# Kernel optimization log

Measured on AMD Instinct MI355X. Metric: run time of the kernel, lower is better.

## Reference

```python
import jax, jax.numpy as jnp
import numpy as np

B, Q, K = 16, 8192, 8192
D_QK, D_V = 64, 64      # raw query/key and value feature dims
H = 8                    # num_heads
DP = 128                 # proj_qks output dim (per default MLP [128, 128])
VP = 64                  # proj_vs output dim (per default MLP [128, 64])
LN_EPS = 1e-6            # flax LayerNorm default


def setup_inputs() -> dict:
    key = jax.random.key(0)
    ks_ = jax.random.split(key, 12)
    f = lambda k, s: jax.random.normal(k, s, jnp.float32)
    return {
        "qs": f(ks_[0], (B, Q, D_QK)),
        "ks": f(ks_[1], (B, K, D_QK)),
        "vs": f(ks_[2], (B, K, D_V)),
        "qs_s": f(ks_[3], (B, Q, D_QK)),
        "ks_s": f(ks_[4], (B, K, D_QK)),
        "valid_lens": jax.random.randint(ks_[5], (B,), 1, K + 1, jnp.int32),
        # proj_qks = MLP([128, 128], gelu): Dense(128) -> gelu -> Dense(128)
        "Wq1": f(ks_[6], (2 * D_QK, DP)) / np.sqrt(2 * D_QK).astype(np.float32),
        "bq1": jnp.zeros((DP,), jnp.float32),
        "Wq2": f(ks_[7], (DP, DP)) / np.sqrt(DP).astype(np.float32),
        "bq2": jnp.zeros((DP,), jnp.float32),
        # proj_vs = MLP([128, 64], gelu): Dense(128) -> gelu -> Dense(64)
        "Wv1": f(ks_[8], (D_V, DP)) / np.sqrt(D_V).astype(np.float32),
        "bv1": jnp.zeros((DP,), jnp.float32),
        "Wv2": f(ks_[9], (DP, VP)) / np.sqrt(DP).astype(np.float32),
        "bv2": jnp.zeros((VP,), jnp.float32),
        "ln_scale": jnp.ones((VP,), jnp.float32),
        "ln_bias": jnp.zeros((VP,), jnp.float32),
    }


def _mlp2(x, W1, b1, W2, b2):
    # Dense -> gelu (tanh approx, flax default) -> Dense
    return jax.nn.gelu(x @ W1 + b1) @ W2 + b2


def reference(qs, ks, vs, qs_s, ks_s, valid_lens,
              Wq1, bq1, Wq2, bq2, Wv1, bv1, Wv2, bv2,
              ln_scale, ln_bias):
    Kl, D = ks.shape[-2], ks.shape[-1]  # D taken BEFORE stacking, as in source
    scale = D ** 0.25
    # stack spatial features then feature-map MLPs
    q = _mlp2(jnp.concatenate([qs_s, qs], axis=-1), Wq1, bq1, Wq2, bq2) / scale
    k = _mlp2(jnp.concatenate([ks_s, ks], axis=-1), Wq1, bq1, Wq2, bq2) / scale
    v = _mlp2(vs, Wv1, bv1, Wv2, bv2)
    # valid-length masking of keys, mean-style normalization of values
    mask = (jnp.arange(Kl)[None, :] < valid_lens[:, None]).astype(k.dtype)[..., None]
    k = k * mask
    v = v / valid_lens[:, None, None].astype(v.dtype)
    Bn, Qn = q.shape[0], q.shape[1]
    q = q.reshape(Bn, Qn, H, DP // H)   # B Q H d
    k = k.reshape(Bn, Kl, H, DP // H)   # B K H d
    v = v.reshape(Bn, Kl, H, VP // H)   # B K H e
    # linear attention: KV outer-product summary then apply queries
    kv = jnp.einsum('bkhd,bkhe->bhde', k, v)          # B H d e
    ctx = jnp.einsum('bqhd,bhde->bqhe', q, kv)        # B Q H e
    ctx = ctx.reshape(Bn, Qn, VP)
    # LayerNorm over last dim
    mu = ctx.mean(-1, keepdims=True)
    var = ((ctx - mu) ** 2).mean(-1, keepdims=True)
    return (ctx - mu) * jax.lax.rsqrt(var + LN_EPS) * ln_scale + ln_bias
```

## Files before the change

kernel.cpp:

```cpp
#include <hip/hip_runtime.h>
#include <hip/hip_bf16.h>


typedef __attribute__((ext_vector_type(8))) short short8;
typedef __attribute__((ext_vector_type(4))) float f32x4;
typedef unsigned int u32;
typedef unsigned short u16;

#define MFMA(A,B,C) __builtin_amdgcn_mfma_f32_16x16x32_bf16((A),(B),(C),0,0,0)
#define SBAR() __builtin_amdgcn_sched_barrier(0)

#define LDH 136
#define LDT 40
#define INVS 0.3535533905932738f

__device__ __forceinline__ u16 bfc(float x){
  __hip_bfloat16 h = __float2bfloat16(x);
  return __bfloat16_as_ushort(h);
}
__device__ __forceinline__ u32 pack2(float a, float b){
  return (u32)bfc(a) | ((u32)bfc(b) << 16);
}
__device__ __forceinline__ float b2f(u16 w){
  return __uint_as_float(((u32)w) << 16);
}
__device__ __forceinline__ short8 cvt8(f32x4 lo, f32x4 hi){
  short8 r;
  r[0]=(short)bfc(lo[0]); r[1]=(short)bfc(lo[1]);
  r[2]=(short)bfc(lo[2]); r[3]=(short)bfc(lo[3]);
  r[4]=(short)bfc(hi[0]); r[5]=(short)bfc(hi[1]);
  r[6]=(short)bfc(hi[2]); r[7]=(short)bfc(hi[3]);
  return r;
}
__device__ __forceinline__ float gelu_f(float x){
  float s = x*x;
  float u = x * __builtin_fmaf(s, 0.035677408136300125f, 0.7978845608028654f);
  float e = __builtin_amdgcn_exp2f(u * -2.885390081777927f);
  return x * __builtin_amdgcn_rcpf(1.0f + e);
}

__global__ void dk_prep(const float* __restrict__ Wq1, const float* __restrict__ Wq2,
                        const float* __restrict__ Wv1, const float* __restrict__ Wv2,
                        u16* __restrict__ wt){
  int i = blockIdx.x*256 + threadIdx.x;
  int e = i & 7;
  int lane = (i >> 3) & 63;
  int chunk = i >> 9;
  int c = lane & 15, g = lane >> 4;
  int k0 = 8*g + e;
  float v;
  if (chunk < 32){
    int mt = chunk >> 2, ks4 = chunk & 3;
    v = Wq1[(ks4*32 + k0)*128 + mt*16 + c];
  } else if (chunk < 64){
    int ch = chunk - 32; int mt = ch >> 2, ks4 = ch & 3;
    v = Wq2[(ks4*32 + k0)*128 + mt*16 + c] * INVS;
  } else if (chunk < 80){
    int ch = chunk - 64; int mt = ch >> 1, ks2 = ch & 1;
    v = Wv1[(ks2*32 + k0)*128 + mt*16 + c];
  } else {
    int ch = chunk - 80; int n2 = ch >> 2, ks4 = ch & 3;
    v = Wv2[(ks4*32 + k0)*64 + n2*16 + c];
  }
  wt[i] = bfc(v);
}

__global__ __launch_bounds__(128, 2) void dk_stage1(
    const float* __restrict__ ksp, const float* __restrict__ kssp,
    const float* __restrict__ vsp, const int* __restrict__ vlen,
    const float* __restrict__ bq1, const float* __restrict__ bq2,
    const float* __restrict__ bv1, const float* __restrict__ bv2,
    const u16* __restrict__ wt, float* __restrict__ kvgr, int repmask)
{
  __shared__ u16 sA[2][5120];
  __shared__ u16 sB[2][2560];
  const int tid = threadIdx.x;
  const int w = tid >> 6, l = tid & 63;
  const int c = l & 15, g = l >> 4;

  int pfx = (l < 16) ? ((vlen[l] + 63) >> 6) : 0;
  #pragma unroll
  for (int m=1; m<16; m<<=1){
    int v = __shfl_up(pfx, m, 64);
    if (l >= m) pfx += v;
  }
  const int T = __shfl(pfx, 15, 64);
  const int t = blockIdx.x;
  if (t >= T) return;
  unsigned long long mk = __ballot(l < 16 && pfx <= t);
  const int b = __popcll(mk);
  const int jb = t - (b ? __shfl(pfx, b-1, 64) : 0);
  const int len = vlen[b];
  const int rbase = jb*64 + w*32;
  if (rbase >= len) return;
  const int rep = t & repmask;
  const size_t row0 = (size_t)b*8192 + rbase;

  u16* H1 = sA[w];
  u16* KT = sA[w];
  u16* VT = sB[w];
  const u16* Wq1t = wt;
  const u16* Wq2t = wt + 16384;
  const u16* Wv1t = wt + 32768;
  const u16* Wv2t = wt + 40960;
  const f32x4 z4 = {0.f,0.f,0.f,0.f};

  {
    f32x4 xvf[8];
    #pragma unroll
    for (int ks2=0; ks2<2; ++ks2){
      #pragma unroll
      for (int nt=0; nt<2; ++nt){
        const float* src = vsp + (row0 + nt*16 + c)*64 + ks2*32 + 8*g;
        xvf[(ks2*2+nt)*2+0] = *(const f32x4*)src;
        xvf[(ks2*2+nt)*2+1] = *(const f32x4*)(src+4);
      }
    }
    SBAR();
    short8 xv[2][2];
    #pragma unroll
    for (int ks2=0; ks2<2; ++ks2)
      #pragma unroll
      for (int nt=0; nt<2; ++nt)
        xv[ks2][nt] = cvt8(xvf[(ks2*2+nt)*2+0], xvf[(ks2*2+nt)*2+1]);
    f32x4 av[8][2];
    #pragma unroll
    for (int mt=0; mt<8; ++mt){ av[mt][0]=z4; av[mt][1]=z4; }
    #pragma unroll
    for (int ks2=0; ks2<2; ++ks2){
      short8 wa[8];
      #pragma unroll
      for (int mt=0; mt<8; ++mt)
        wa[mt] = *(const short8*)&Wv1t[((mt*2+ks2)*64 + l)*8];
      SBAR();
      #pragma unroll
      for (int mt=0; mt<8; ++mt){
        av[mt][0] = MFMA(wa[mt], xv[ks2][0], av[mt][0]);
        av[mt][1] = MFMA(wa[mt], xv[ks2][1], av[mt][1]);
      }
    }
    #pragma unroll
    for (int mt=0; mt<8; ++mt){
      const f32x4 bia = *(const f32x4*)&bv1[mt*16 + 4*g];
      #pragma unroll
      for (int nt=0; nt<2; ++nt){
        uint2 pp;
        pp.x = pack2(gelu_f(av[mt][nt][0]+bia[0]), gelu_f(av[mt][nt][1]+bia[1]));
        pp.y = pack2(gelu_f(av[mt][nt][2]+bia[2]), gelu_f(av[mt][nt][3]+bia[3]));
        *(uint2*)&H1[(nt*16 + c)*LDH + mt*16 + 4*g] = pp;
      }
    }
  }
  {
    f32x4 acv[2][4];
    #pragma unroll
    for (int n2=0; n2<4; ++n2){ acv[0][n2]=z4; acv[1][n2]=z4; }
    #pragma unroll
    for (int ks4=0; ks4<4; ++ks4){
      short8 wb[4];
      #pragma unroll
      for (int n2=0; n2<4; ++n2)
        wb[n2] = *(const short8*)&Wv2t[((n2*4+ks4)*64 + l)*8];
      SBAR();
      const short8 ah0 = *(const short8*)&H1[(c     )*LDH + ks4*32 + 8*g];
      const short8 ah1 = *(const short8*)&H1[(16 + c)*LDH + ks4*32 + 8*g];
      #pragma unroll
      for (int n2=0; n2<4; ++n2){
        acv[0][n2] = MFMA(ah0, wb[n2], acv[0][n2]);
        acv[1][n2] = MFMA(ah1, wb[n2], acv[1][n2]);
      }
    }
    #pragma unroll
    for (int n2=0; n2<4; ++n2){
      const float bb = bv2[n2*16 + c];
      #pragma unroll
      for (int mt=0; mt<2; ++mt){
        uint2 pp;
        pp.x = pack2(acv[mt][n2][0]+bb, acv[mt][n2][1]+bb);
        pp.y = pack2(acv[mt][n2][2]+bb, acv[mt][n2][3]+bb);
        *(uint2*)&VT[(n2*16+c)*LDT + mt*16 + 4*g] = pp;
      }
    }
  }
  {
    f32x4 xkf[16];
    #pragma unroll
    for (int ks4=0; ks4<4; ++ks4){
      #pragma unroll
      for (int nt=0; nt<2; ++nt){
        const int kk = ks4*32 + 8*g;
        const float* src = (ks4 < 2) ? (kssp + (row0 + nt*16 + c)*64 + kk)
                                     : (ksp  + (row0 + nt*16 + c)*64 + (kk - 64));
        xkf[(ks4*2+nt)*2+0] = *(const f32x4*)src;
        xkf[(ks4*2+nt)*2+1] = *(const f32x4*)(src+4);
      }
    }
    SBAR();
    short8 xk[4][2];
    #pragma unroll
    for (int ks4=0; ks4<4; ++ks4)
      #pragma unroll
      for (int nt=0; nt<2; ++nt)
        xk[ks4][nt] = cvt8(xkf[(ks4*2+nt)*2+0], xkf[(ks4*2+nt)*2+1]);
    f32x4 acc[8][2];
    #pragma unroll
    for (int mt=0; mt<8; ++mt){ acc[mt][0]=z4; acc[mt][1]=z4; }
    #pragma unroll
    for (int ks4=0; ks4<4; ++ks4){
      short8 wa[8];
      #pragma unroll
      for (int mt=0; mt<8; ++mt)
        wa[mt] = *(const short8*)&Wq1t[((mt*4+ks4)*64 + l)*8];
      SBAR();
      #pragma unroll
      for (int mt=0; mt<8; ++mt){
        acc[mt][0] = MFMA(wa[mt], xk[ks4][0], acc[mt][0]);
        acc[mt][1] = MFMA(wa[mt], xk[ks4][1], acc[mt][1]);
      }
    }
    #pragma unroll
    for (int mt=0; mt<8; ++mt){
      const f32x4 bia = *(const f32x4*)&bq1[mt*16 + 4*g];
      #pragma unroll
      for (int nt=0; nt<2; ++nt){
        uint2 pp;
        pp.x = pack2(gelu_f(acc[mt][nt][0]+bia[0]), gelu_f(acc[mt][nt][1]+bia[1]));
        pp.y = pack2(gelu_f(acc[mt][nt][2]+bia[2]), gelu_f(acc[mt][nt][3]+bia[3]));
        *(uint2*)&H1[(nt*16 + c)*LDH + mt*16 + 4*g] = pp;
      }
    }
  }
  {
    f32x4 acc2[2][8];
    #pragma unroll
    for (int n2=0; n2<8; ++n2){ acc2[0][n2]=z4; acc2[1][n2]=z4; }
    #pragma unroll
    for (int ks4=0; ks4<4; ++ks4){
      short8 wb[8];
      #pragma unroll
      for (int n2=0; n2<8; ++n2)
        wb[n2] = *(const short8*)&Wq2t[((n2*4+ks4)*64 + l)*8];
      SBAR();
      const short8 ah0 = *(const short8*)&H1[(c     )*LDH + ks4*32 + 8*g];
      const short8 ah1 = *(const short8*)&H1[(16 + c)*LDH + ks4*32 + 8*g];
      #pragma unroll
      for (int n2=0; n2<8; ++n2){
        acc2[0][n2] = MFMA(ah0, wb[n2], acc2[0][n2]);
        acc2[1][n2] = MFMA(ah1, wb[n2], acc2[1][n2]);
      }
    }
    #pragma unroll
    for (int n2=0; n2<8; ++n2){
      const float bb = bq2[n2*16 + c] * INVS;
      #pragma unroll
      for (int mt=0; mt<2; ++mt){
        const int r0 = rbase + mt*16 + 4*g;
        float v0 = (r0+0 < len) ? acc2[mt][n2][0] + bb : 0.f;
        float v1 = (r0+1 < len) ? acc2[mt][n2][1] + bb : 0.f;
        float v2 = (r0+2 < len) ? acc2[mt][n2][2] + bb : 0.f;
        float v3 = (r0+3 < len) ? acc2[mt][n2][3] + bb : 0.f;
        uint2 pp; pp.x = pack2(v0,v1); pp.y = pack2(v2,v3);
        *(uint2*)&KT[(n2*16 + c)*LDT + mt*16 + 4*g] = pp;
      }
    }
  }
  {
    short8 zf = {0,0,0,0,0,0,0,0};
    f32x4 kvacc[8];
    #pragma unroll
    for (int h=0; h<8; ++h) kvacc[h] = z4;
    #pragma unroll
    for (int h=0; h<8; ++h){
      const short8 ka = *(const short8*)&KT[(h*16 + c)*LDT + 8*g];
      short8 vb = zf;
      if (c < 8) vb = *(const short8*)&VT[(h*8 + c)*LDT + 8*g];
      kvacc[h] = MFMA(ka, vb, kvacc[h]);
    }
    if (c < 8){
      float* kvg = kvgr + ((size_t)rep*16 + b)*1024;
      #pragma unroll
      for (int h=0; h<8; ++h){
        #pragma unroll
        for (int r=0; r<4; ++r)
          atomicAdd(&kvg[(h*16 + 4*g + r)*8 + c], kvacc[h][r]);
      }
    }
  }
}

__global__ void dk_mid(const float* __restrict__ kvgr, int nrep,
                       const int* __restrict__ vlen,
                       const float* __restrict__ bq2,
                       const u16* __restrict__ wt,
                       u16* __restrict__ Mt, float* __restrict__ c0g)
{
  __shared__ float kvs[1024];
  const int b = blockIdx.x, t = threadIdx.x;
  const float inv_len = 1.0f / (float)vlen[b];
  #pragma unroll
  for (int k=0; k<4; ++k){
    const int idx = t + 256*k;
    float s = 0.f;
    for (int r=0; r<nrep; ++r) s += kvgr[((size_t)r*16 + b)*1024 + idx];
    kvs[idx] = s * inv_len;
  }
  __syncthreads();
  for (int k=0; k<32; ++k){
    const int o = t + 256*k;
    const int e = o >> 7, j = o & 127;
    const int h = e >> 3, e8 = e & 7;
    const int ks4 = j >> 5, gg = (j >> 3) & 3, el = j & 7;
    float s = 0.f;
    #pragma unroll
    for (int d=0; d<16; ++d){
      const int od = h*16 + d;
      const u16 wv = wt[16384 + (((od>>4)*4 + ks4)*64 + gg*16 + (od&15))*8 + el];
      s += b2f(wv) * kvs[h*128 + d*8 + e8];
    }
    const int n3 = e >> 4, cc = e & 15;
    Mt[(size_t)b*8192 + ((n3*4 + ks4)*64 + gg*16 + cc)*8 + el] = bfc(s);
  }
  if (t < 64){
    const int e = t, h = e >> 3, e8 = e & 7;
    float s = 0.f;
    #pragma unroll
    for (int d=0; d<16; ++d)
      s += bq2[h*16+d] * INVS * kvs[h*128 + d*8 + e8];
    c0g[b*64 + e] = s;
  }
}

__global__ __launch_bounds__(128, 2) void dk_stage2(
    const float* __restrict__ qsp, const float* __restrict__ qssp,
    const float* __restrict__ bq1,
    const float* __restrict__ lnw_g, const float* __restrict__ lnb_g,
    const u16* __restrict__ wt, const u16* __restrict__ Mt,
    const float* __restrict__ c0g, float* __restrict__ outp)
{
  __shared__ u16 sH1[2][32*LDH];
  const int tid = threadIdx.x;
  const int w = tid >> 6, l = tid & 63;
  const int c = l & 15, g = l >> 4;
  const int b  = blockIdx.x >> 7;
  const int jb = blockIdx.x & 127;
  const int rbase = jb*64 + w*32;
  u16* H1 = sH1[w];
  const u16* Wq1t = wt;
  const size_t row0 = (size_t)b*8192 + rbase;
  const f32x4 z4 = {0.f,0.f,0.f,0.f};

  {
    f32x4 xqf[16];
    #pragma unroll
    for (int ks4=0; ks4<4; ++ks4){
      #pragma unroll
      for (int nt=0; nt<2; ++nt){
        const int kk = ks4*32 + 8*g;
        const float* src = (ks4 < 2) ? (qssp + (row0 + nt*16 + c)*64 + kk)
                                     : (qsp  + (row0 + nt*16 + c)*64 + (kk - 64));
        xqf[(ks4*2+nt)*2+0] = *(const f32x4*)src;
        xqf[(ks4*2+nt)*2+1] = *(const f32x4*)(src+4);
      }
    }
    SBAR();
    short8 xq[4][2];
    #pragma unroll
    for (int ks4=0; ks4<4; ++ks4)
      #pragma unroll
      for (int nt=0; nt<2; ++nt)
        xq[ks4][nt] = cvt8(xqf[(ks4*2+nt)*2+0], xqf[(ks4*2+nt)*2+1]);
    f32x4 acc[8][2];
    #pragma unroll
    for (int mt=0; mt<8; ++mt){ acc[mt][0]=z4; acc[mt][1]=z4; }
    #pragma unroll
    for (int ks4=0; ks4<4; ++ks4){
      short8 wa[8];
      #pragma unroll
      for (int mt=0; mt<8; ++mt)
        wa[mt] = *(const short8*)&Wq1t[((mt*4+ks4)*64 + l)*8];
      SBAR();
      #pragma unroll
      for (int mt=0; mt<8; ++mt){
        acc[mt][0] = MFMA(wa[mt], xq[ks4][0], acc[mt][0]);
        acc[mt][1] = MFMA(wa[mt], xq[ks4][1], acc[mt][1]);
      }
    }
    #pragma unroll
    for (int mt=0; mt<8; ++mt){
      const f32x4 bia = *(const f32x4*)&bq1[mt*16 + 4*g];
      #pragma unroll
      for (int nt=0; nt<2; ++nt){
        uint2 pp;
        pp.x = pack2(gelu_f(acc[mt][nt][0]+bia[0]), gelu_f(acc[mt][nt][1]+bia[1]));
        pp.y = pack2(gelu_f(acc[mt][nt][2]+bia[2]), gelu_f(acc[mt][nt][3]+bia[3]));
        *(uint2*)&H1[(nt*16 + c)*LDH + mt*16 + 4*g] = pp;
      }
    }
  }
  f32x4 acc3[2][4];
  #pragma unroll
  for (int n3=0; n3<4; ++n3){ acc3[0][n3]=z4; acc3[1][n3]=z4; }
  const u16* Mb = Mt + (size_t)b*8192;
  {
    short8 bm[16];
    #pragma unroll
    for (int ks4=0; ks4<4; ++ks4)
      #pragma unroll
      for (int n3=0; n3<4; ++n3)
        bm[ks4*4+n3] = *(const short8*)&Mb[((n3*4+ks4)*64 + l)*8];
    SBAR();
    #pragma unroll
    for (int ks4=0; ks4<4; ++ks4){
      const short8 aq0 = *(const short8*)&H1[(c     )*LDH + ks4*32 + 8*g];
      const short8 aq1 = *(const short8*)&H1[(16 + c)*LDH + ks4*32 + 8*g];
      #pragma unroll
      for (int n3=0; n3<4; ++n3){
        acc3[0][n3] = MFMA(aq0, bm[ks4*4+n3], acc3[0][n3]);
        acc3[1][n3] = MFMA(aq1, bm[ks4*4+n3], acc3[1][n3]);
      }
    }
  }
  float c0v[4];
  #pragma unroll
  for (int n3=0; n3<4; ++n3) c0v[n3] = c0g[b*64 + n3*16 + c];
  float lnw[4], lnb[4];
  #pragma unroll
  for (int n3=0; n3<4; ++n3){ lnw[n3] = lnw_g[n3*16 + c]; lnb[n3] = lnb_g[n3*16 + c]; }
  float* Tb = (float*)H1;
  #pragma unroll
  for (int mt=0; mt<2; ++mt){
    #pragma unroll
    for (int r=0; r<4; ++r){
      float s1 = 0.f, s2 = 0.f;
      #pragma unroll
      for (int n3=0; n3<4; ++n3){
        float v = acc3[mt][n3][r] + c0v[n3];
        s1 += v; s2 += v*v;
      }
      #pragma unroll
      for (int m=1; m<16; m<<=1){
        s1 += __shfl_xor(s1, m, 64);
        s2 += __shfl_xor(s2, m, 64);
      }
      const float mu = s1 * (1.0f/64.0f);
      const float var = s2 * (1.0f/64.0f) - mu*mu;
      const float rs = rsqrtf(var + 1e-6f);
      const int rloc = mt*16 + 4*g + r;
      #pragma unroll
      for (int n3=0; n3<4; ++n3)
        Tb[rloc*68 + n3*16 + c] = (acc3[mt][n3][r] + c0v[n3] - mu)*rs*lnw[n3] + lnb[n3];
    }
  }
  float* ob = outp + row0*64;
  #pragma unroll
  for (int i=0; i<8; ++i){
    const int row = i*4 + (l>>4);
    const f32x4 vv = *(const f32x4*)&Tb[row*68 + (l&15)*4];
    *(f32x4*)(ob + row*64 + (l&15)*4) = vv;
  }
}

extern "C" void kernel_launch(void* const* d_in, const int* in_sizes, int n_in,
                              void* d_out, int out_size, void* d_ws, size_t ws_size,
                              hipStream_t stream)
{
  const float* qs   = (const float*)d_in[0];
  const float* ks   = (const float*)d_in[1];
  const float* vs   = (const float*)d_in[2];
  const float* qs_s = (const float*)d_in[3];
  const float* ks_s = (const float*)d_in[4];
  const int*   vl   = (const int*)d_in[5];
  const float* Wq1  = (const float*)d_in[6];
  const float* bq1  = (const float*)d_in[7];
  const float* Wq2  = (const float*)d_in[8];
  const float* bq2  = (const float*)d_in[9];
  const float* Wv1  = (const float*)d_in[10];
  const float* bv1  = (const float*)d_in[11];
  const float* Wv2  = (const float*)d_in[12];
  const float* bv2  = (const float*)d_in[13];
  const float* lnw  = (const float*)d_in[14];
  const float* lnb  = (const float*)d_in[15];
  (void)in_sizes; (void)n_in; (void)out_size;

  const size_t fixed = 96*1024 + 256*1024 + 4096;
  int nrep = 4;
  while (nrep > 1 && (size_t)nrep*65536 + fixed > ws_size) nrep >>= 1;
  float* kvgr = (float*)d_ws;
  u16*   wt   = (u16*)((char*)d_ws + (size_t)nrep*65536);
  u16*   Mt   = (u16*)((char*)wt + 96*1024);
  float* c0   = (float*)((char*)Mt + 256*1024);

  hipMemsetAsync(kvgr, 0, (size_t)nrep*65536, stream);
  dk_prep<<<192, 256, 0, stream>>>(Wq1, Wq2, Wv1, Wv2, wt);
  dk_stage1<<<2048, 128, 0, stream>>>(ks, ks_s, vs, vl, bq1, bq2, bv1, bv2,
                                      wt, kvgr, nrep - 1);
  dk_mid<<<16, 256, 0, stream>>>(kvgr, nrep, vl, bq2, wt, Mt, c0);
  dk_stage2<<<2048, 128, 0, stream>>>(qs, qs_s, bq1, lnw, lnb, wt, Mt, c0,
                                      (float*)d_out);
}
```

Baseline: 92.17 us.

## Stage bf16 weight tiles in shared memory cooperatively per block

Both kernels now copy each weight matrix (Wv1/Wv2, then Wq1, then Wq2) from global memory into a 32KB shared buffer using both waves cooperatively. Each wave then reads its MFMA operand fragments from LDS instead of global/L2, which halves the per-block global weight traffic. In stage2 the loads of the M matrix are hoisted to the top to overlap with the input and weight loads. The early per-wave return was removed so that __syncthreads is safe. The cost is extra LDS use (lower occupancy headroom), extra barriers, and more register pressure from the staging buffers.

```diff
diff --git a/kernel.cpp b/kernel.cpp
--- a/kernel.cpp
+++ b/kernel.cpp
@@ -74,6 +74,7 @@
 {
   __shared__ u16 sA[2][5120];
   __shared__ u16 sB[2][2560];
+  __shared__ u16 sW[16384];
   const int tid = threadIdx.x;
   const int w = tid >> 6, l = tid & 63;
   const int c = l & 15, g = l >> 4;
@@ -92,20 +93,19 @@
   const int jb = t - (b ? __shfl(pfx, b-1, 64) : 0);
   const int len = vlen[b];
   const int rbase = jb*64 + w*32;
-  if (rbase >= len) return;
   const int rep = t & repmask;
   const size_t row0 = (size_t)b*8192 + rbase;
 
   u16* H1 = sA[w];
   u16* KT = sA[w];
   u16* VT = sB[w];
-  const u16* Wq1t = wt;
-  const u16* Wq2t = wt + 16384;
-  const u16* Wv1t = wt + 32768;
-  const u16* Wv2t = wt + 40960;
   const f32x4 z4 = {0.f,0.f,0.f,0.f};
 
   {
+    uint4 stg[16];
+    #pragma unroll
+    for (int j=0; j<16; ++j)
+      stg[j] = *(const uint4*)&wt[((size_t)(64 + j*2 + w)*64 + l)*8];
     f32x4 xvf[8];
     #pragma unroll
     for (int ks2=0; ks2<2; ++ks2){
@@ -117,6 +117,11 @@
       }
     }
     SBAR();
+    #pragma unroll
+    for (int j=0; j<16; ++j)
+      *(uint4*)&sW[((j*2 + w)*64 + l)*8] = stg[j];
+    __syncthreads();
+
     short8 xv[2][2];
     #pragma unroll
     for (int ks2=0; ks2<2; ++ks2)
@@ -131,7 +136,7 @@
       short8 wa[8];
       #pragma unroll
       for (int mt=0; mt<8; ++mt)
-        wa[mt] = *(const short8*)&Wv1t[((mt*2+ks2)*64 + l)*8];
+        wa[mt] = *(const short8*)&sW[((mt*2+ks2)*64 + l)*8];
       SBAR();
       #pragma unroll
       for (int mt=0; mt<8; ++mt){
@@ -150,8 +155,6 @@
         *(uint2*)&H1[(nt*16 + c)*LDH + mt*16 + 4*g] = pp;
       }
     }
-  }
-  {
     f32x4 acv[2][4];
     #pragma unroll
     for (int n2=0; n2<4; ++n2){ acv[0][n2]=z4; acv[1][n2]=z4; }
@@ -160,7 +163,7 @@
       short8 wb[4];
       #pragma unroll
       for (int n2=0; n2<4; ++n2)
-        wb[n2] = *(const short8*)&Wv2t[((n2*4+ks4)*64 + l)*8];
+        wb[n2] = *(const short8*)&sW[((16 + n2*4+ks4)*64 + l)*8];
       SBAR();
       const short8 ah0 = *(const short8*)&H1[(c     )*LDH + ks4*32 + 8*g];
       const short8 ah1 = *(const short8*)&H1[(16 + c)*LDH + ks4*32 + 8*g];
@@ -182,7 +185,14 @@
       }
     }
   }
+  __syncthreads();
+
+  short8 xk[4][2];
   {
+    uint4 stg[16];
+    #pragma unroll
+    for (int j=0; j<16; ++j)
+      stg[j] = *(const uint4*)&wt[((size_t)(j*2 + w)*64 + l)*8];
     f32x4 xkf[16];
     #pragma unroll
     for (int ks4=0; ks4<4; ++ks4){
@@ -196,7 +206,11 @@
       }
     }
     SBAR();
-    short8 xk[4][2];
+    #pragma unroll
+    for (int j=0; j<16; ++j)
+      *(uint4*)&sW[((j*2 + w)*64 + l)*8] = stg[j];
+    __syncthreads();
+
     #pragma unroll
     for (int ks4=0; ks4<4; ++ks4)
       #pragma unroll
@@ -210,7 +224,7 @@
       short8 wa[8];
       #pragma unroll
       for (int mt=0; mt<8; ++mt)
-        wa[mt] = *(const short8*)&Wq1t[((mt*4+ks4)*64 + l)*8];
+        wa[mt] = *(const short8*)&sW[((mt*4+ks4)*64 + l)*8];
       SBAR();
       #pragma unroll
       for (int mt=0; mt<8; ++mt){
@@ -230,7 +244,19 @@
       }
     }
   }
+  __syncthreads();
+
   {
+    uint4 stg[16];
+    #pragma unroll
+    for (int j=0; j<16; ++j)
+      stg[j] = *(const uint4*)&wt[((size_t)(32 + j*2 + w)*64 + l)*8];
+    SBAR();
+    #pragma unroll
+    for (int j=0; j<16; ++j)
+      *(uint4*)&sW[((j*2 + w)*64 + l)*8] = stg[j];
+    __syncthreads();
+
     f32x4 acc2[2][8];
     #pragma unroll
     for (int n2=0; n2<8; ++n2){ acc2[0][n2]=z4; acc2[1][n2]=z4; }
@@ -239,7 +265,7 @@
       short8 wb[8];
       #pragma unroll
       for (int n2=0; n2<8; ++n2)
-        wb[n2] = *(const short8*)&Wq2t[((n2*4+ks4)*64 + l)*8];
+        wb[n2] = *(const short8*)&sW[((n2*4+ks4)*64 + l)*8];
       SBAR();
       const short8 ah0 = *(const short8*)&H1[(c     )*LDH + ks4*32 + 8*g];
       const short8 ah1 = *(const short8*)&H1[(16 + c)*LDH + ks4*32 + 8*g];
@@ -263,8 +289,6 @@
         *(uint2*)&KT[(n2*16 + c)*LDT + mt*16 + 4*g] = pp;
       }
     }
-  }
-  {
     short8 zf = {0,0,0,0,0,0,0,0};
     f32x4 kvacc[8];
     #pragma unroll
@@ -338,6 +362,7 @@
     const float* __restrict__ c0g, float* __restrict__ outp)
 {
   __shared__ u16 sH1[2][32*LDH];
+  __shared__ u16 sW[16384];
   const int tid = threadIdx.x;
   const int w = tid >> 6, l = tid & 63;
   const int c = l & 15, g = l >> 4;
@@ -345,24 +370,39 @@
   const int jb = blockIdx.x & 127;
   const int rbase = jb*64 + w*32;
   u16* H1 = sH1[w];
-  const u16* Wq1t = wt;
   const size_t row0 = (size_t)b*8192 + rbase;
   const f32x4 z4 = {0.f,0.f,0.f,0.f};
+  const u16* Mb = Mt + (size_t)b*8192;
+
+  uint4 stg[16];
+  #pragma unroll
+  for (int j=0; j<16; ++j)
+    stg[j] = *(const uint4*)&wt[((size_t)(j*2 + w)*64 + l)*8];
+  f32x4 xqf[16];
+  #pragma unroll
+  for (int ks4=0; ks4<4; ++ks4){
+    #pragma unroll
+    for (int nt=0; nt<2; ++nt){
+      const int kk = ks4*32 + 8*g;
+      const float* src = (ks4 < 2) ? (qssp + (row0 + nt*16 + c)*64 + kk)
+                                   : (qsp  + (row0 + nt*16 + c)*64 + (kk - 64));
+      xqf[(ks4*2+nt)*2+0] = *(const f32x4*)src;
+      xqf[(ks4*2+nt)*2+1] = *(const f32x4*)(src+4);
+    }
+  }
+  short8 bm[16];
+  #pragma unroll
+  for (int ks4=0; ks4<4; ++ks4)
+    #pragma unroll
+    for (int n3=0; n3<4; ++n3)
+      bm[ks4*4+n3] = *(const short8*)&Mb[((n3*4+ks4)*64 + l)*8];
+  SBAR();
+  #pragma unroll
+  for (int j=0; j<16; ++j)
+    *(uint4*)&sW[((j*2 + w)*64 + l)*8] = stg[j];
+  __syncthreads();
 
   {
-    f32x4 xqf[16];
-    #pragma unroll
-    for (int ks4=0; ks4<4; ++ks4){
-      #pragma unroll
-      for (int nt=0; nt<2; ++nt){
-        const int kk = ks4*32 + 8*g;
-        const float* src = (ks4 < 2) ? (qssp + (row0 + nt*16 + c)*64 + kk)
-                                     : (qsp  + (row0 + nt*16 + c)*64 + (kk - 64));
-        xqf[(ks4*2+nt)*2+0] = *(const f32x4*)src;
-        xqf[(ks4*2+nt)*2+1] = *(const f32x4*)(src+4);
-      }
-    }
-    SBAR();
     short8 xq[4][2];
     #pragma unroll
     for (int ks4=0; ks4<4; ++ks4)
@@ -377,7 +417,7 @@
       short8 wa[8];
       #pragma unroll
       for (int mt=0; mt<8; ++mt)
-        wa[mt] = *(const short8*)&Wq1t[((mt*4+ks4)*64 + l)*8];
+        wa[mt] = *(const short8*)&sW[((mt*4+ks4)*64 + l)*8];
       SBAR();
       #pragma unroll
       for (int mt=0; mt<8; ++mt){
@@ -400,24 +440,14 @@
   f32x4 acc3[2][4];
   #pragma unroll
   for (int n3=0; n3<4; ++n3){ acc3[0][n3]=z4; acc3[1][n3]=z4; }
-  const u16* Mb = Mt + (size_t)b*8192;
-  {
-    short8 bm[16];
-    #pragma unroll
-    for (int ks4=0; ks4<4; ++ks4)
-      #pragma unroll
-      for (int n3=0; n3<4; ++n3)
-        bm[ks4*4+n3] = *(const short8*)&Mb[((n3*4+ks4)*64 + l)*8];
-    SBAR();
-    #pragma unroll
-    for (int ks4=0; ks4<4; ++ks4){
-      const short8 aq0 = *(const short8*)&H1[(c     )*LDH + ks4*32 + 8*g];
-      const short8 aq1 = *(const short8*)&H1[(16 + c)*LDH + ks4*32 + 8*g];
-      #pragma unroll
-      for (int n3=0; n3<4; ++n3){
-        acc3[0][n3] = MFMA(aq0, bm[ks4*4+n3], acc3[0][n3]);
-        acc3[1][n3] = MFMA(aq1, bm[ks4*4+n3], acc3[1][n3]);
-      }
+  #pragma unroll
+  for (int ks4=0; ks4<4; ++ks4){
+    const short8 aq0 = *(const short8*)&H1[(c     )*LDH + ks4*32 + 8*g];
+    const short8 aq1 = *(const short8*)&H1[(16 + c)*LDH + ks4*32 + 8*g];
+    #pragma unroll
+    for (int n3=0; n3<4; ++n3){
+      acc3[0][n3] = MFMA(aq0, bm[ks4*4+n3], acc3[0][n3]);
+      acc3[1][n3] = MFMA(aq1, bm[ks4*4+n3], acc3[1][n3]);
     }
   }
   float c0v[4];
```

Measured after the change: 126.9 us. +37.6%, slower.

## Stage MLP weights into LDS via double-buffered async global_load_lds

Applied to the files above, without the earlier changes.

Weight fragments used by the MFMA loops were read by every wave straight from global memory. They are now copied into a shared double buffer with global_load_lds, both waves of a block cooperating, and the next chunk is prefetched while the current one is consumed, in both stage1 and stage2. The packed weight layout in the prep kernel is reordered so each 8-chunk group is contiguous in consumption order, and the stage1 early exit for fully masked waves is dropped so block-wide barriers stay valid. This adds several __syncthreads per tile and 16KB of LDS per block, which may reduce occupancy, and masked waves now do redundant work.

```diff
diff --git a/kernel.cpp b/kernel.cpp
--- a/kernel.cpp
+++ b/kernel.cpp
@@ -38,6 +38,19 @@
   float e = __builtin_amdgcn_exp2f(u * -2.885390081777927f);
   return x * __builtin_amdgcn_rcpf(1.0f + e);
 }
+__device__ __forceinline__ void gld_lds16(const u16* gsrc, u16* ldst){
+  __builtin_amdgcn_global_load_lds(
+      (const __attribute__((address_space(1))) void*)gsrc,
+      (__attribute__((address_space(3))) void*)ldst, 16, 0, 0);
+}
+__device__ __forceinline__ void stage8(const u16* __restrict__ wt, u16* dst,
+                                       int chunk0, int w, int l){
+  #pragma unroll
+  for (int j=0; j<4; ++j){
+    const int ch = w*4 + j;
+    gld_lds16(wt + ((size_t)(chunk0 + ch)*64 + l)*8, dst + (size_t)ch*512);
+  }
+}
 
 __global__ void dk_prep(const float* __restrict__ Wq1, const float* __restrict__ Wq2,
                         const float* __restrict__ Wv1, const float* __restrict__ Wv2,
@@ -46,21 +59,21 @@
   int e = i & 7;
   int lane = (i >> 3) & 63;
   int chunk = i >> 9;
-  int c = lane & 15, g = lane >> 4;
-  int k0 = 8*g + e;
+  int c = lane & 15, gg = lane >> 4;
+  int k0 = 8*gg + e;
   float v;
-  if (chunk < 32){
-    int mt = chunk >> 2, ks4 = chunk & 3;
+  if (chunk < 16){
+    int ks2 = chunk >> 3, mt = chunk & 7;
+    v = Wv1[(ks2*32 + k0)*128 + mt*16 + c];
+  } else if (chunk < 32){
+    int j = chunk - 16; int ks4 = j >> 2, n2 = j & 3;
+    v = Wv2[(ks4*32 + k0)*64 + n2*16 + c];
+  } else if (chunk < 64){
+    int j = chunk - 32; int ks4 = j >> 3, mt = j & 7;
     v = Wq1[(ks4*32 + k0)*128 + mt*16 + c];
-  } else if (chunk < 64){
-    int ch = chunk - 32; int mt = ch >> 2, ks4 = ch & 3;
-    v = Wq2[(ks4*32 + k0)*128 + mt*16 + c] * INVS;
-  } else if (chunk < 80){
-    int ch = chunk - 64; int mt = ch >> 1, ks2 = ch & 1;
-    v = Wv1[(ks2*32 + k0)*128 + mt*16 + c];
   } else {
-    int ch = chunk - 80; int n2 = ch >> 2, ks4 = ch & 3;
-    v = Wv2[(ks4*32 + k0)*64 + n2*16 + c];
+    int j = chunk - 64; int ks4 = j >> 3, n2 = j & 7;
+    v = Wq2[(ks4*32 + k0)*128 + n2*16 + c] * INVS;
   }
   wt[i] = bfc(v);
 }
@@ -74,6 +87,7 @@
 {
   __shared__ u16 sA[2][5120];
   __shared__ u16 sB[2][2560];
+  __shared__ u16 sW[2][4096];
   const int tid = threadIdx.x;
   const int w = tid >> 6, l = tid & 63;
   const int c = l & 15, g = l >> 4;
@@ -92,176 +106,208 @@
   const int jb = t - (b ? __shfl(pfx, b-1, 64) : 0);
   const int len = vlen[b];
   const int rbase = jb*64 + w*32;
-  if (rbase >= len) return;
   const int rep = t & repmask;
   const size_t row0 = (size_t)b*8192 + rbase;
 
   u16* H1 = sA[w];
   u16* KT = sA[w];
   u16* VT = sB[w];
-  const u16* Wq1t = wt;
-  const u16* Wq2t = wt + 16384;
-  const u16* Wv1t = wt + 32768;
-  const u16* Wv2t = wt + 40960;
+  u16* W0 = &sW[0][0];
+  u16* W1 = &sW[1][0];
   const f32x4 z4 = {0.f,0.f,0.f,0.f};
 
+  f32x4 xvf[8];
+  #pragma unroll
+  for (int ks2=0; ks2<2; ++ks2){
+    #pragma unroll
+    for (int nt=0; nt<2; ++nt){
+      const float* src = vsp + (row0 + nt*16 + c)*64 + ks2*32 + 8*g;
+      xvf[(ks2*2+nt)*2+0] = *(const f32x4*)src;
+      xvf[(ks2*2+nt)*2+1] = *(const f32x4*)(src+4);
+    }
+  }
+  stage8(wt, W0, 0, w, l);
+  SBAR();
+  __syncthreads();
+
+  short8 xv[2][2];
+  #pragma unroll
+  for (int ks2=0; ks2<2; ++ks2)
+    #pragma unroll
+    for (int nt=0; nt<2; ++nt)
+      xv[ks2][nt] = cvt8(xvf[(ks2*2+nt)*2+0], xvf[(ks2*2+nt)*2+1]);
+
+  f32x4 av[8][2];
+  #pragma unroll
+  for (int mt=0; mt<8; ++mt){ av[mt][0]=z4; av[mt][1]=z4; }
+  stage8(wt, W1, 8, w, l);
   {
-    f32x4 xvf[8];
-    #pragma unroll
-    for (int ks2=0; ks2<2; ++ks2){
-      #pragma unroll
-      for (int nt=0; nt<2; ++nt){
-        const float* src = vsp + (row0 + nt*16 + c)*64 + ks2*32 + 8*g;
-        xvf[(ks2*2+nt)*2+0] = *(const f32x4*)src;
-        xvf[(ks2*2+nt)*2+1] = *(const f32x4*)(src+4);
-      }
-    }
-    SBAR();
-    short8 xv[2][2];
-    #pragma unroll
-    for (int ks2=0; ks2<2; ++ks2)
-      #pragma unroll
-      for (int nt=0; nt<2; ++nt)
-        xv[ks2][nt] = cvt8(xvf[(ks2*2+nt)*2+0], xvf[(ks2*2+nt)*2+1]);
-    f32x4 av[8][2];
-    #pragma unroll
-    for (int mt=0; mt<8; ++mt){ av[mt][0]=z4; av[mt][1]=z4; }
-    #pragma unroll
-    for (int ks2=0; ks2<2; ++ks2){
-      short8 wa[8];
-      #pragma unroll
-      for (int mt=0; mt<8; ++mt)
-        wa[mt] = *(const short8*)&Wv1t[((mt*2+ks2)*64 + l)*8];
-      SBAR();
-      #pragma unroll
-      for (int mt=0; mt<8; ++mt){
-        av[mt][0] = MFMA(wa[mt], xv[ks2][0], av[mt][0]);
-        av[mt][1] = MFMA(wa[mt], xv[ks2][1], av[mt][1]);
-      }
-    }
+    short8 wa[8];
+    #pragma unroll
+    for (int mt=0; mt<8; ++mt) wa[mt] = *(const short8*)&W0[(mt*64 + l)*8];
+    SBAR();
     #pragma unroll
     for (int mt=0; mt<8; ++mt){
-      const f32x4 bia = *(const f32x4*)&bv1[mt*16 + 4*g];
-      #pragma unroll
-      for (int nt=0; nt<2; ++nt){
-        uint2 pp;
-        pp.x = pack2(gelu_f(av[mt][nt][0]+bia[0]), gelu_f(av[mt][nt][1]+bia[1]));
-        pp.y = pack2(gelu_f(av[mt][nt][2]+bia[2]), gelu_f(av[mt][nt][3]+bia[3]));
-        *(uint2*)&H1[(nt*16 + c)*LDH + mt*16 + 4*g] = pp;
-      }
-    }
-  }
+      av[mt][0] = MFMA(wa[mt], xv[0][0], av[mt][0]);
+      av[mt][1] = MFMA(wa[mt], xv[0][1], av[mt][1]);
+    }
+  }
+  __syncthreads();
+  stage8(wt, W0, 16, w, l);
   {
-    f32x4 acv[2][4];
-    #pragma unroll
-    for (int n2=0; n2<4; ++n2){ acv[0][n2]=z4; acv[1][n2]=z4; }
-    #pragma unroll
-    for (int ks4=0; ks4<4; ++ks4){
-      short8 wb[4];
-      #pragma unroll
-      for (int n2=0; n2<4; ++n2)
-        wb[n2] = *(const short8*)&Wv2t[((n2*4+ks4)*64 + l)*8];
-      SBAR();
-      const short8 ah0 = *(const short8*)&H1[(c     )*LDH + ks4*32 + 8*g];
-      const short8 ah1 = *(const short8*)&H1[(16 + c)*LDH + ks4*32 + 8*g];
-      #pragma unroll
-      for (int n2=0; n2<4; ++n2){
-        acv[0][n2] = MFMA(ah0, wb[n2], acv[0][n2]);
-        acv[1][n2] = MFMA(ah1, wb[n2], acv[1][n2]);
-      }
-    }
+    short8 wa[8];
+    #pragma unroll
+    for (int mt=0; mt<8; ++mt) wa[mt] = *(const short8*)&W1[(mt*64 + l)*8];
+    SBAR();
+    #pragma unroll
+    for (int mt=0; mt<8; ++mt){
+      av[mt][0] = MFMA(wa[mt], xv[1][0], av[mt][0]);
+      av[mt][1] = MFMA(wa[mt], xv[1][1], av[mt][1]);
+    }
+  }
+  #pragma unroll
+  for (int mt=0; mt<8; ++mt){
+    const f32x4 bia = *(const f32x4*)&bv1[mt*16 + 4*g];
+    #pragma unroll
+    for (int nt=0; nt<2; ++nt){
+      uint2 pp;
+      pp.x = pack2(gelu_f(av[mt][nt][0]+bia[0]), gelu_f(av[mt][nt][1]+bia[1]));
+      pp.y = pack2(gelu_f(av[mt][nt][2]+bia[2]), gelu_f(av[mt][nt][3]+bia[3]));
+      *(uint2*)&H1[(nt*16 + c)*LDH + mt*16 + 4*g] = pp;
+    }
+  }
+  __syncthreads();
+
+  f32x4 acv[2][4];
+  #pragma unroll
+  for (int n2=0; n2<4; ++n2){ acv[0][n2]=z4; acv[1][n2]=z4; }
+  stage8(wt, W1, 24, w, l);
+  #pragma unroll
+  for (int ks4=0; ks4<2; ++ks4){
+    short8 wb[4];
+    #pragma unroll
+    for (int n2=0; n2<4; ++n2) wb[n2] = *(const short8*)&W0[((ks4*4+n2)*64 + l)*8];
+    SBAR();
+    const short8 ah0 = *(const short8*)&H1[(c     )*LDH + ks4*32 + 8*g];
+    const short8 ah1 = *(const short8*)&H1[(16 + c)*LDH + ks4*32 + 8*g];
     #pragma unroll
     for (int n2=0; n2<4; ++n2){
-      const float bb = bv2[n2*16 + c];
-      #pragma unroll
-      for (int mt=0; mt<2; ++mt){
-        uint2 pp;
-        pp.x = pack2(acv[mt][n2][0]+bb, acv[mt][n2][1]+bb);
-        pp.y = pack2(acv[mt][n2][2]+bb, acv[mt][n2][3]+bb);
-        *(uint2*)&VT[(n2*16+c)*LDT + mt*16 + 4*g] = pp;
-      }
-    }
-  }
-  {
-    f32x4 xkf[16];
-    #pragma unroll
-    for (int ks4=0; ks4<4; ++ks4){
-      #pragma unroll
-      for (int nt=0; nt<2; ++nt){
-        const int kk = ks4*32 + 8*g;
-        const float* src = (ks4 < 2) ? (kssp + (row0 + nt*16 + c)*64 + kk)
-                                     : (ksp  + (row0 + nt*16 + c)*64 + (kk - 64));
-        xkf[(ks4*2+nt)*2+0] = *(const f32x4*)src;
-        xkf[(ks4*2+nt)*2+1] = *(const f32x4*)(src+4);
-      }
-    }
-    SBAR();
-    short8 xk[4][2];
-    #pragma unroll
-    for (int ks4=0; ks4<4; ++ks4)
-      #pragma unroll
-      for (int nt=0; nt<2; ++nt)
-        xk[ks4][nt] = cvt8(xkf[(ks4*2+nt)*2+0], xkf[(ks4*2+nt)*2+1]);
-    f32x4 acc[8][2];
-    #pragma unroll
-    for (int mt=0; mt<8; ++mt){ acc[mt][0]=z4; acc[mt][1]=z4; }
-    #pragma unroll
-    for (int ks4=0; ks4<4; ++ks4){
-      short8 wa[8];
-      #pragma unroll
-      for (int mt=0; mt<8; ++mt)
-        wa[mt] = *(const short8*)&Wq1t[((mt*4+ks4)*64 + l)*8];
-      SBAR();
-      #pragma unroll
-      for (int mt=0; mt<8; ++mt){
-        acc[mt][0] = MFMA(wa[mt], xk[ks4][0], acc[mt][0]);
-        acc[mt][1] = MFMA(wa[mt], xk[ks4][1], acc[mt][1]);
-      }
-    }
+      acv[0][n2] = MFMA(ah0, wb[n2], acv[0][n2]);
+      acv[1][n2] = MFMA(ah1, wb[n2], acv[1][n2]);
+    }
+  }
+  __syncthreads();
+  stage8(wt, W0, 32, w, l);
+  f32x4 xkf[16];
+  #pragma unroll
+  for (int ks4=0; ks4<4; ++ks4){
+    #pragma unroll
+    for (int nt=0; nt<2; ++nt){
+      const int kk = ks4*32 + 8*g;
+      const float* src = (ks4 < 2) ? (kssp + (row0 + nt*16 + c)*64 + kk)
+                                   : (ksp  + (row0 + nt*16 + c)*64 + (kk - 64));
+      xkf[(ks4*2+nt)*2+0] = *(const f32x4*)src;
+      xkf[(ks4*2+nt)*2+1] = *(const f32x4*)(src+4);
+    }
+  }
+  SBAR();
+  #pragma unroll
+  for (int ks4=2; ks4<4; ++ks4){
+    short8 wb[4];
+    #pragma unroll
+    for (int n2=0; n2<4; ++n2) wb[n2] = *(const short8*)&W1[(((ks4-2)*4+n2)*64 + l)*8];
+    SBAR();
+    const short8 ah0 = *(const short8*)&H1[(c     )*LDH + ks4*32 + 8*g];
+    const short8 ah1 = *(const short8*)&H1[(16 + c)*LDH + ks4*32 + 8*g];
+    #pragma unroll
+    for (int n2=0; n2<4; ++n2){
+      acv[0][n2] = MFMA(ah0, wb[n2], acv[0][n2]);
+      acv[1][n2] = MFMA(ah1, wb[n2], acv[1][n2]);
+    }
+  }
+  #pragma unroll
+  for (int n2=0; n2<4; ++n2){
+    const float bb = bv2[n2*16 + c];
+    #pragma unroll
+    for (int mt=0; mt<2; ++mt){
+      uint2 pp;
+      pp.x = pack2(acv[mt][n2][0]+bb, acv[mt][n2][1]+bb);
+      pp.y = pack2(acv[mt][n2][2]+bb, acv[mt][n2][3]+bb);
+      *(uint2*)&VT[(n2*16+c)*LDT + mt*16 + 4*g] = pp;
+    }
+  }
+  __syncthreads();
+
+  short8 xk[4][2];
+  #pragma unroll
+  for (int ks4=0; ks4<4; ++ks4)
+    #pragma unroll
+    for (int nt=0; nt<2; ++nt)
+      xk[ks4][nt] = cvt8(xkf[(ks4*2+nt)*2+0], xkf[(ks4*2+nt)*2+1]);
+  f32x4 acc[8][2];
+  #pragma unroll
+  for (int mt=0; mt<8; ++mt){ acc[mt][0]=z4; acc[mt][1]=z4; }
+  #pragma unroll
+  for (int i=0; i<4; ++i){
+    u16* rd = (i & 1) ? W1 : W0;
+    u16* wr = (i & 1) ? W0 : W1;
+    stage8(wt, wr, 40 + 8*i, w, l);
+    short8 wa[8];
+    #pragma unroll
+    for (int mt=0; mt<8; ++mt) wa[mt] = *(const short8*)&rd[(mt*64 + l)*8];
+    SBAR();
     #pragma unroll
     for (int mt=0; mt<8; ++mt){
-      const f32x4 bia = *(const f32x4*)&bq1[mt*16 + 4*g];
-      #pragma unroll
-      for (int nt=0; nt<2; ++nt){
-        uint2 pp;
-        pp.x = pack2(gelu_f(acc[mt][nt][0]+bia[0]), gelu_f(acc[mt][nt][1]+bia[1]));
-        pp.y = pack2(gelu_f(acc[mt][nt][2]+bia[2]), gelu_f(acc[mt][nt][3]+bia[3]));
-        *(uint2*)&H1[(nt*16 + c)*LDH + mt*16 + 4*g] = pp;
-      }
-    }
-  }
-  {
-    f32x4 acc2[2][8];
-    #pragma unroll
-    for (int n2=0; n2<8; ++n2){ acc2[0][n2]=z4; acc2[1][n2]=z4; }
-    #pragma unroll
-    for (int ks4=0; ks4<4; ++ks4){
-      short8 wb[8];
-      #pragma unroll
-      for (int n2=0; n2<8; ++n2)
-        wb[n2] = *(const short8*)&Wq2t[((n2*4+ks4)*64 + l)*8];
-      SBAR();
-      const short8 ah0 = *(const short8*)&H1[(c     )*LDH + ks4*32 + 8*g];
-      const short8 ah1 = *(const short8*)&H1[(16 + c)*LDH + ks4*32 + 8*g];
-      #pragma unroll
-      for (int n2=0; n2<8; ++n2){
-        acc2[0][n2] = MFMA(ah0, wb[n2], acc2[0][n2]);
-        acc2[1][n2] = MFMA(ah1, wb[n2], acc2[1][n2]);
-      }
-    }
+      acc[mt][0] = MFMA(wa[mt], xk[i][0], acc[mt][0]);
+      acc[mt][1] = MFMA(wa[mt], xk[i][1], acc[mt][1]);
+    }
+    __syncthreads();
+  }
+  #pragma unroll
+  for (int mt=0; mt<8; ++mt){
+    const f32x4 bia = *(const f32x4*)&bq1[mt*16 + 4*g];
+    #pragma unroll
+    for (int nt=0; nt<2; ++nt){
+      uint2 pp;
+      pp.x = pack2(gelu_f(acc[mt][nt][0]+bia[0]), gelu_f(acc[mt][nt][1]+bia[1]));
+      pp.y = pack2(gelu_f(acc[mt][nt][2]+bia[2]), gelu_f(acc[mt][nt][3]+bia[3]));
+      *(uint2*)&H1[(nt*16 + c)*LDH + mt*16 + 4*g] = pp;
+    }
+  }
+
+  f32x4 acc2[2][8];
+  #pragma unroll
+  for (int n2=0; n2<8; ++n2){ acc2[0][n2]=z4; acc2[1][n2]=z4; }
+  #pragma unroll
+  for (int i=0; i<4; ++i){
+    u16* rd = (i & 1) ? W1 : W0;
+    u16* wr = (i & 1) ? W0 : W1;
+    if (i < 3) stage8(wt, wr, 72 + 8*i, w, l);
+    short8 wb[8];
+    #pragma unroll
+    for (int n2=0; n2<8; ++n2) wb[n2] = *(const short8*)&rd[(n2*64 + l)*8];
+    SBAR();
+    const short8 ah0 = *(const short8*)&H1[(c     )*LDH + i*32 + 8*g];
+    const short8 ah1 = *(const short8*)&H1[(16 + c)*LDH + i*32 + 8*g];
     #pragma unroll
     for (int n2=0; n2<8; ++n2){
-      const float bb = bq2[n2*16 + c] * INVS;
-      #pragma unroll
-      for (int mt=0; mt<2; ++mt){
-        const int r0 = rbase + mt*16 + 4*g;
-        float v0 = (r0+0 < len) ? acc2[mt][n2][0] + bb : 0.f;
-        float v1 = (r0+1 < len) ? acc2[mt][n2][1] + bb : 0.f;
-        float v2 = (r0+2 < len) ? acc2[mt][n2][2] + bb : 0.f;
-        float v3 = (r0+3 < len) ? acc2[mt][n2][3] + bb : 0.f;
-        uint2 pp; pp.x = pack2(v0,v1); pp.y = pack2(v2,v3);
-        *(uint2*)&KT[(n2*16 + c)*LDT + mt*16 + 4*g] = pp;
-      }
+      acc2[0][n2] = MFMA(ah0, wb[n2], acc2[0][n2]);
+      acc2[1][n2] = MFMA(ah1, wb[n2], acc2[1][n2]);
+    }
+    if (i < 3) __syncthreads();
+  }
+  #pragma unroll
+  for (int n2=0; n2<8; ++n2){
+    const float bb = bq2[n2*16 + c] * INVS;
+    #pragma unroll
+    for (int mt=0; mt<2; ++mt){
+      const int r0 = rbase + mt*16 + 4*g;
+      float v0 = (r0+0 < len) ? acc2[mt][n2][0] + bb : 0.f;
+      float v1 = (r0+1 < len) ? acc2[mt][n2][1] + bb : 0.f;
+      float v2 = (r0+2 < len) ? acc2[mt][n2][2] + bb : 0.f;
+      float v3 = (r0+3 < len) ? acc2[mt][n2][3] + bb : 0.f;
+      uint2 pp; pp.x = pack2(v0,v1); pp.y = pack2(v2,v3);
+      *(uint2*)&KT[(n2*16 + c)*LDT + mt*16 + 4*g] = pp;
     }
   }
   {
@@ -314,7 +360,7 @@
     #pragma unroll
     for (int d=0; d<16; ++d){
       const int od = h*16 + d;
-      const u16 wv = wt[16384 + (((od>>4)*4 + ks4)*64 + gg*16 + (od&15))*8 + el];
+      const u16 wv = wt[((size_t)(64 + ks4*8 + (od>>4))*64 + gg*16 + (od&15))*8 + el];
       s += b2f(wv) * kvs[h*128 + d*8 + e8];
     }
     const int n3 = e >> 4, cc = e & 15;
@@ -338,6 +384,7 @@
     const float* __restrict__ c0g, float* __restrict__ outp)
 {
   __shared__ u16 sH1[2][32*LDH];
+  __shared__ u16 sW[2][4096];
   const int tid = threadIdx.x;
   const int w = tid >> 6, l = tid & 63;
   const int c = l & 15, g = l >> 4;
@@ -345,62 +392,67 @@
   const int jb = blockIdx.x & 127;
   const int rbase = jb*64 + w*32;
   u16* H1 = sH1[w];
-  const u16* Wq1t = wt;
+  u16* W0 = &sW[0][0];
+  u16* W1 = &sW[1][0];
   const size_t row0 = (size_t)b*8192 + rbase;
   const f32x4 z4 = {0.f,0.f,0.f,0.f};
-
-  {
-    f32x4 xqf[16];
-    #pragma unroll
-    for (int ks4=0; ks4<4; ++ks4){
-      #pragma unroll
-      for (int nt=0; nt<2; ++nt){
-        const int kk = ks4*32 + 8*g;
-        const float* src = (ks4 < 2) ? (qssp + (row0 + nt*16 + c)*64 + kk)
-                                     : (qsp  + (row0 + nt*16 + c)*64 + (kk - 64));
-        xqf[(ks4*2+nt)*2+0] = *(const f32x4*)src;
-        xqf[(ks4*2+nt)*2+1] = *(const f32x4*)(src+4);
-      }
-    }
-    SBAR();
-    short8 xq[4][2];
-    #pragma unroll
-    for (int ks4=0; ks4<4; ++ks4)
-      #pragma unroll
-      for (int nt=0; nt<2; ++nt)
-        xq[ks4][nt] = cvt8(xqf[(ks4*2+nt)*2+0], xqf[(ks4*2+nt)*2+1]);
-    f32x4 acc[8][2];
-    #pragma unroll
-    for (int mt=0; mt<8; ++mt){ acc[mt][0]=z4; acc[mt][1]=z4; }
-    #pragma unroll
-    for (int ks4=0; ks4<4; ++ks4){
-      short8 wa[8];
-      #pragma unroll
-      for (int mt=0; mt<8; ++mt)
-        wa[mt] = *(const short8*)&Wq1t[((mt*4+ks4)*64 + l)*8];
-      SBAR();
-      #pragma unroll
-      for (int mt=0; mt<8; ++mt){
-        acc[mt][0] = MFMA(wa[mt], xq[ks4][0], acc[mt][0]);
-        acc[mt][1] = MFMA(wa[mt], xq[ks4][1], acc[mt][1]);
-      }
-    }
+  const u16* Mb = Mt + (size_t)b*8192;
+
+  f32x4 xqf[16];
+  #pragma unroll
+  for (int ks4=0; ks4<4; ++ks4){
+    #pragma unroll
+    for (int nt=0; nt<2; ++nt){
+      const int kk = ks4*32 + 8*g;
+      const float* src = (ks4 < 2) ? (qssp + (row0 + nt*16 + c)*64 + kk)
+                                   : (qsp  + (row0 + nt*16 + c)*64 + (kk - 64));
+      xqf[(ks4*2+nt)*2+0] = *(const f32x4*)src;
+      xqf[(ks4*2+nt)*2+1] = *(const f32x4*)(src+4);
+    }
+  }
+  stage8(wt, W0, 32, w, l);
+  SBAR();
+  __syncthreads();
+
+  short8 xq[4][2];
+  #pragma unroll
+  for (int ks4=0; ks4<4; ++ks4)
+    #pragma unroll
+    for (int nt=0; nt<2; ++nt)
+      xq[ks4][nt] = cvt8(xqf[(ks4*2+nt)*2+0], xqf[(ks4*2+nt)*2+1]);
+  f32x4 acc[8][2];
+  #pragma unroll
+  for (int mt=0; mt<8; ++mt){ acc[mt][0]=z4; acc[mt][1]=z4; }
+  #pragma unroll
+  for (int i=0; i<4; ++i){
+    u16* rd = (i & 1) ? W1 : W0;
+    u16* wr = (i & 1) ? W0 : W1;
+    if (i < 3) stage8(wt, wr, 32 + 8*(i+1), w, l);
+    short8 wa[8];
+    #pragma unroll
+    for (int mt=0; mt<8; ++mt) wa[mt] = *(const short8*)&rd[(mt*64 + l)*8];
+    SBAR();
     #pragma unroll
     for (int mt=0; mt<8; ++mt){
-      const f32x4 bia = *(const f32x4*)&bq1[mt*16 + 4*g];
-      #pragma unroll
-      for (int nt=0; nt<2; ++nt){
-        uint2 pp;
-        pp.x = pack2(gelu_f(acc[mt][nt][0]+bia[0]), gelu_f(acc[mt][nt][1]+bia[1]));
-        pp.y = pack2(gelu_f(acc[mt][nt][2]+bia[2]), gelu_f(acc[mt][nt][3]+bia[3]));
-        *(uint2*)&H1[(nt*16 + c)*LDH + mt*16 + 4*g] = pp;
-      }
+      acc[mt][0] = MFMA(wa[mt], xq[i][0], acc[mt][0]);
+      acc[mt][1] = MFMA(wa[mt], xq[i][1], acc[mt][1]);
+    }
+    if (i < 3) __syncthreads();
+  }
+  #pragma unroll
+  for (int mt=0; mt<8; ++mt){
+    const f32x4 bia = *(const f32x4*)&bq1[mt*16 + 4*g];
+    #pragma unroll
+    for (int nt=0; nt<2; ++nt){
+      uint2 pp;
+      pp.x = pack2(gelu_f(acc[mt][nt][0]+bia[0]), gelu_f(acc[mt][nt][1]+bia[1]));
+      pp.y = pack2(gelu_f(acc[mt][nt][2]+bia[2]), gelu_f(acc[mt][nt][3]+bia[3]));
+      *(uint2*)&H1[(nt*16 + c)*LDH + mt*16 + 4*g] = pp;
     }
   }
   f32x4 acc3[2][4];
   #pragma unroll
   for (int n3=0; n3<4; ++n3){ acc3[0][n3]=z4; acc3[1][n3]=z4; }
-  const u16* Mb = Mt + (size_t)b*8192;
   {
     short8 bm[16];
     #pragma unroll
```

Measured after the change: 106.2 us. 1.15x slower.
